# Kernel optimization log

Measured on AMD Instinct MI355X. Metric: run time of the kernel, lower is better.

The kernel has to match this reference:

```python
import jax, jax.numpy as jnp
import numpy as np

B, NJ, NW, NT, D, H = 1024, 16, 2, 2, 128, 128


def _mlp2(x, W1, b1, W2, b2):
    # two-layer dense net with relu on every layer (edge/node networks)
    return jax.nn.relu(jax.nn.relu(x @ W1 + b1) @ W2 + b2)


def _edge_block(src, dst, W1, b1, W2, b2, mask_dst=None):
    # fully-connected edge block: edge(i,j) = MLP(concat(src_i, dst_j)),
    # then avg-pool over destination nodes (masked if mask_dst given)
    Bb, Ns, ds = src.shape
    Nd, dd = dst.shape[1], dst.shape[2]
    e_in = jnp.concatenate([
        jnp.broadcast_to(src[:, :, None, :], (Bb, Ns, Nd, ds)),
        jnp.broadcast_to(dst[:, None, :, :], (Bb, Ns, Nd, dd)),
    ], axis=-1)                              # [B, Ns, Nd, 2D]
    h = _mlp2(e_in, W1, b1, W2, b2)          # [B, Ns, Nd, H]
    if mask_dst is not None:
        m = mask_dst.astype(h.dtype)[:, None, :, None]
        pooled = (h * m).sum(axis=2) / jnp.maximum(m.sum(axis=2), 1.0)
    else:
        pooled = h.mean(axis=2)
    return pooled                            # [B, Ns, H]


def setup_inputs() -> dict:
    key = jax.random.key(0)
    ks = jax.random.split(key, 10)
    def w(k, shape, fan_in):
        return jax.random.normal(k, shape, jnp.float32) / np.float32(np.sqrt(fan_in))
    return {
        "jets": jax.random.normal(ks[0], (B, NJ, D), jnp.float32),
        "nodes_w": jax.random.normal(ks[1], (B, NW, D), jnp.float32),
        "nodes_top": jax.random.normal(ks[2], (B, NT, D), jnp.float32),
        "mask": jax.random.bernoulli(ks[3], 0.8, (B, NJ)),
        # 7 edge nets: 0 jet-jet, 1 jet-W, 2 jet-top, 3 W-jet, 4 W-top, 5 top-jet, 6 top-W
        "edge_W1": w(ks[4], (7, 2 * D, H), 2 * D),
        "edge_b1": jnp.zeros((7, H), jnp.float32),
        "edge_W2": w(ks[5], (7, H, H), H),
        "edge_b2": jnp.zeros((7, H), jnp.float32),
        # jet node net: input D + 3H
        "jet_W1": w(ks[6], (D + 3 * H, H), D + 3 * H),
        "jet_b1": jnp.zeros((H,), jnp.float32),
        "jet_W2": w(ks[7], (H, H), H),
        "jet_b2": jnp.zeros((H,), jnp.float32),
        # W / top node nets (stacked): input D + 2H
        "wt_W1": w(ks[8], (2, D + 2 * H, H), D + 2 * H),
        "wt_b1": jnp.zeros((2, H), jnp.float32),
        "wt_W2": w(ks[9], (2, H, H), H),
        "wt_b2": jnp.zeros((2, H), jnp.float32),
    }


def reference(jets, nodes_w, nodes_top, mask,
              edge_W1, edge_b1, edge_W2, edge_b2,
              jet_W1, jet_b1, jet_W2, jet_b2,
              wt_W1, wt_b1, wt_W2, wt_b2):
    eb = lambda i, s, d, m: _edge_block(s, d, edge_W1[i], edge_b1[i], edge_W2[i], edge_b2[i], m)
    mf = mask.astype(jets.dtype)
    # --- jet update ---
    p_jj = eb(0, jets, jets, mask)
    p_jw = eb(1, jets, nodes_w, None)
    p_jt = eb(2, jets, nodes_top, None)
    jets_cat = jnp.concatenate([jets, p_jj, p_jw, p_jt], axis=-1)
    jets_out = _mlp2(jets_cat, jet_W1, jet_b1, jet_W2, jet_b2) * mf[..., None]
    # --- W update ---
    p_wj = eb(3, nodes_w, jets, mask)
    p_wt = eb(4, nodes_w, nodes_top, None)
    ws_out = _mlp2(jnp.concatenate([nodes_w, p_wj, p_wt], axis=-1),
                   wt_W1[0], wt_b1[0], wt_W2[0], wt_b2[0])
    # --- top update ---
    p_tj = eb(5, nodes_top, jets, mask)
    p_tw = eb(6, nodes_top, nodes_w, None)
    tops_out = _mlp2(jnp.concatenate([nodes_top, p_tj, p_tw], axis=-1),
                     wt_W1[1], wt_b1[1], wt_W2[1], wt_b2[1])
    # concat all updated node types along the node axis: [B, NJ+NW+NT, H]
    return jnp.concatenate([jets_out, ws_out, tops_out], axis=1)
```

## Files before the change

kernel.cpp:

```cpp
#include <hip/hip_runtime.h>
#include <hip/hip_bf16.h>


using short4v = __attribute__((ext_vector_type(4))) short;
using short8 = __attribute__((ext_vector_type(8))) short;
using f32x4  = __attribute__((ext_vector_type(4))) float;
using u32x4  = __attribute__((ext_vector_type(4))) unsigned;

#define DEVI __device__ __forceinline__

DEVI float b2f(short s){
  unsigned u = ((unsigned)(unsigned short)s) << 16;
  float f; __builtin_memcpy(&f, &u, 4); return f;
}
DEVI float lo16f(unsigned w){ unsigned u = w << 16; float f; __builtin_memcpy(&f,&u,4); return f; }
DEVI float hi16f(unsigned w){ unsigned u = w & 0xffff0000u; float f; __builtin_memcpy(&f,&u,4); return f; }
DEVI short f2b(float f){
  __hip_bfloat16 h = __float2bfloat16(f);
  short s; __builtin_memcpy(&s, &h, 2); return s;
}
DEVI unsigned cvtpk(float lo, float hi){
  unsigned r;
  asm("v_cvt_pk_bf16_f32 %0, %1, %2" : "=v"(r) : "v"(lo), "v"(hi));
  return r;
}
DEVI float ldflex(const void* p, long i, int bf){
  return bf ? b2f(((const short*)p)[i]) : ((const float*)p)[i];
}
DEVI f32x4 mfma16(short8 a, short8 b, f32x4 c){
  return __builtin_amdgcn_mfma_f32_16x16x32_bf16(a, b, c, 0, 0, 0);
}

DEVI int detect_bf(const void* jets){
  int l = threadIdx.x & 63;
  int extreme = 0;
  #pragma unroll
  for(int s=0;s<4;s++){
    unsigned short v = ((const unsigned short*)jets)[(l*4+s)*2];
    int e = (v>>7)&0xff;
    if(e<110||e>140) extreme++;
  }
  #pragma unroll
  for(int o=1;o<64;o<<=1) extreme += __shfl_xor(extreme, o);
  return (extreme <= 32) ? 1 : 0;
}
DEVI int detect_fmt(const void* mask){
  int l = threadIdx.x & 63;
  bool all01=true, allf32=true;
  #pragma unroll
  for(int s=0;s<4;s++){
    unsigned w = ((const unsigned*)mask)[l*4+s];
    if(w>1u) all01=false;
    if(w!=0u && w!=0x3F800000u) allf32=false;
  }
  bool allbfv=true; int evnz=0;
  #pragma unroll
  for(int s=0;s<8;s++){
    unsigned short v = ((const unsigned short*)mask)[l*8+s];
    if(v!=0&&v!=0x3F80) allbfv=false;
    if(((l*8+s)&1)==0 && v!=0) evnz++;
  }
  #pragma unroll
  for(int o=1;o<64;o<<=1) evnz += __shfl_xor(evnz, o);
  bool allb01=true;
  #pragma unroll
  for(int s=0;s<16;s++){ if(((const unsigned char*)mask)[l*16+s]>1) allb01=false; }
  int a01 = __all(all01), af32 = __all(allf32), abf = __all(allbfv), ab01 = __all(allb01);
  int fmt = 0;
  if(a01) fmt=0; else if(abf && evnz>0) fmt=2; else if(af32) fmt=3; else if(ab01) fmt=1;
  return fmt;
}

constexpr size_t OF_MASKF  = 256;
constexpr size_t OF_INVCNT = 65792;
constexpr size_t OF_XJ     = 69888;
constexpr size_t OF_XW     = 4264192;
constexpr size_t OF_XT     = 4788480;
constexpr size_t OF_W1T    = 5312768;
constexpr size_t OF_W2T    = 5771520;
constexpr size_t OF_EB1F   = 6000896;
constexpr size_t OF_EB2F   = 6004480;
constexpr size_t OF_JW1T   = 6008064;
constexpr size_t OF_JW2T   = 6139136;
constexpr size_t OF_JB1F   = 6171904;
constexpr size_t OF_JB2F   = 6172416;
constexpr size_t OF_WTW1T  = 6172928;
constexpr size_t OF_WTW2T  = 6369536;
constexpr size_t OF_WTB1F  = 6435072;
constexpr size_t OF_WTB2F  = 6436096;
constexpr size_t OF_UVJ    = 6437120;
constexpr size_t OF_UVW    = 31602944;
constexpr size_t OF_UVT    = 33700096;
constexpr size_t OF_POOL   = 65157376;

__constant__ int QJ_NET[14]  = {0,0,1,2,3,5, 1,3,4,6, 2,4,5,6};
__constant__ int QJ_HALF[14] = {0,1,0,0,1,1, 1,0,0,1, 1,1,0,0};
__constant__ int EB_CUM[8] = {0,2048,2304,2560,2816,3072,3104,3136};
__constant__ int EB_NET[7] = {0,1,2,3,5,4,6};
__constant__ int EN_LGRPB[7] = {8,5,5,5,2,5,2};
__constant__ int EN_LGND2[7] = {4,1,1,4,1,4,1};
__constant__ int EN_LGNSB[7] = {4,4,4,1,1,1,1};
__constant__ int EN_USEL[7] = {0,0,0,1,1,2,2};
__constant__ long long EN_UOFF[7] = {0,4194304,6291456,262144,524288,524288,786432};
__constant__ int EN_VSEL[7] = {0,1,2,0,2,0,1};
__constant__ long long EN_VOFF[7] = {2097152,0,0,8388608,262144,10485760,786432};
__constant__ long long EN_POOL[7] = {0,2097152,4194304,6291456,6553600,6815744,7077888};
__constant__ int TJ_CUM[21] = {0,32,64,96,128,160,192,224,240,256,272,288,304,320,336,400,416,464,512,528,544};
__constant__ int TJ_SEL[20] = {0,0,0,0,0,0,0,1,1,1,1,1,1,1,2,3,4,4,5,5};
__constant__ int TJ_OFF[20] = {0,32768,65536,98304,131072,163840,196608,
                               0,16384,32768,49152,65536,81920,98304,
                               0,0,0,49152,0,16384};
__constant__ int TJ_R[20]   = {256,256,256,256,256,256,256,128,128,128,128,128,128,128,512,128,384,384,128,128};

__global__ __launch_bounds__(256) void k_prep(
    const void* jets, const void* nw, const void* ntop, const void* mask,
    const void* eW1, const void* eb1, const void* eW2, const void* eb2,
    const void* jW1, const void* jb1, const void* jW2, const void* jb2,
    const void* wW1, const void* wb1, const void* wW2, const void* wb2,
    int* flags, float* maskf, float* invcnt,
    short* XJ, short* XW, short* XT,
    short* W1T, short* W2T, short* JW1T, short* JW2T, short* WTW1T, short* WTW2T,
    float* EB1F, float* EB2F, float* JB1F, float* JB2F, float* WTB1F, float* WTB2F){
  __shared__ float tl[32][33];
  int bid = blockIdx.x;
  if(bid < 2560){
    int bf = detect_bf(jets);
    long i = ((long)bid*256 + threadIdx.x)*4;
    const void* src; short* dst; long o;
    if(i < 2097152){ src=jets; dst=XJ; o=i; }
    else if(i < 2359296){ src=nw; dst=XW; o=i-2097152; }
    else { src=ntop; dst=XT; o=i-2359296; }
    short4v r;
    if(bf){
      r = *(const short4v*)((const short*)src + o);
    } else {
      f32x4 v = *(const f32x4*)((const float*)src + o);
      #pragma unroll
      for(int e=0;e<4;e++) r[e] = f2b(v[e]);
    }
    *(short4v*)(dst + o) = r;
  } else if(bid < 3104){
    int bf = detect_bf(jets);
    int tile = bid - 2560; int job = 0;
    while(tile >= TJ_CUM[job+1]) job++;
    tile -= TJ_CUM[job];
    int sel = TJ_SEL[job]; long off = TJ_OFF[job]; int R = TJ_R[job];
    const void* src = sel==0?eW1: sel==1?eW2: sel==2?jW1: sel==3?jW2: sel==4?wW1: wW2;
    short* dst = sel==0?W1T: sel==1?W2T: sel==2?JW1T: sel==3?JW2T: sel==4?WTW1T: WTW2T;
    int tr = (tile>>2)*32, tc = (tile&3)*32;
    int t = threadIdx.x, r = t>>3, c4 = (t&7)*4;
    #pragma unroll
    for(int j=0;j<4;j++) tl[r][c4+j] = ldflex(src, off + (long)(tr+r)*128 + tc + c4 + j, bf);
    __syncthreads();
    short4v o;
    #pragma unroll
    for(int j=0;j<4;j++) o[j] = f2b(tl[c4+j][r]);
    *(short4v*)(dst + off + (long)(tc+r)*R + tr + c4) = o;
  } else if(bid < 3168){
    int fmt = detect_fmt(mask);
    int t = (bid-3104)*256 + threadIdx.x;
    float m;
    if(fmt==0)      m = (((const int*)mask)[t]!=0) ? 1.f : 0.f;
    else if(fmt==1) m = (((const unsigned char*)mask)[t]!=0) ? 1.f : 0.f;
    else if(fmt==2) m = (b2f(((const short*)mask)[t])!=0.f) ? 1.f : 0.f;
    else            m = (((const float*)mask)[t]!=0.f) ? 1.f : 0.f;
    maskf[t] = m;
    float s = m;
    for(int o=1;o<16;o<<=1) s += __shfl_xor(s, o);
    if((t&15)==0) invcnt[t>>4] = 1.f / fmaxf(s, 1.f);
  } else if(bid < 3178){
    int bf = detect_bf(jets);
    int id = (bid-3168)*256 + threadIdx.x;
    if(id<896)        EB1F[id]       = ldflex(eb1, id, bf);
    else if(id<1792)  EB2F[id-896]   = ldflex(eb2, id-896, bf);
    else if(id<1920)  JB1F[id-1792]  = ldflex(jb1, id-1792, bf);
    else if(id<2048)  JB2F[id-1920]  = ldflex(jb2, id-1920, bf);
    else if(id<2304)  WTB1F[id-2048] = ldflex(wb1, id-2048, bf);
    else if(id<2560)  WTB2F[id-2304] = ldflex(wb2, id-2304, bf);
  } else {
    if(threadIdx.x < 64){
      int bf = detect_bf(jets);
      int fmt = detect_fmt(mask);
      if((threadIdx.x & 63) == 0){ flags[0] = bf; flags[1] = fmt; }
    }
  }
}

__global__ __launch_bounds__(256, 4) void k_proj(const short* XJ, const short* XW, const short* XT,
    const short* W1T, const float* EB1F, short* UVJ, short* UVW, short* UVT){
  int bid = blockIdx.x;
  int jp, rb; const short* X; short* out;
  if(bid < 768){ jp = bid>>7; rb = bid&127; X=XJ; out=UVJ + jp*2097152; }
  else if(bid < 832){ int r2=bid-768; jp = 6 + (r2>>4); rb = r2&15; X=XW; out=UVW + (jp-6)*262144; }
  else { int r2=bid-832; jp = 10 + (r2>>4); rb = r2&15; X=XT; out=UVT + (jp-10)*262144; }
  int net = QJ_NET[jp], half = QJ_HALF[jp];
  bool addb = (half==0);
  long row0 = (long)rb * 128;
  const short* Wb = W1T + net*32768 + half*128;
  int t = threadIdx.x, lane = t & 63, wv = t >> 6;
  int rbw = wv >> 1, ch = (wv & 1)*64;
  int cl = lane & 15, kh = lane >> 4;
  short8 bw[4][4];
  f32x4 biasv[4];
  #pragma unroll
  for(int nt=0;nt<4;nt++){
    #pragma unroll
    for(int ks=0;ks<4;ks++)
      bw[nt][ks] = *(const short8*)(Wb + (ch + nt*16 + cl)*256 + ks*32 + kh*8);
    if(addb) biasv[nt] = *(const f32x4*)(EB1F + net*128 + ch + nt*16 + kh*4);
    else     biasv[nt] = f32x4{0.f,0.f,0.f,0.f};
  }
  #pragma unroll 1
  for(int c=0;c<4;c++){
    long T0 = row0 + c*32 + rbw*16;
    short8 a[4];
    #pragma unroll
    for(int ks=0;ks<4;ks++)
      a[ks] = *(const short8*)(X + (T0 + cl)*128 + ks*32 + kh*8);
    f32x4 acc[4] = {};
    #pragma unroll
    for(int ks=0;ks<4;ks++)
      #pragma unroll
      for(int nt=0;nt<4;nt++)
        acc[nt] = mfma16(bw[nt][ks], a[ks], acc[nt]);
    #pragma unroll
    for(int nt=0;nt<4;nt++){
      short4v sv;
      #pragma unroll
      for(int r=0;r<4;r++) sv[r] = f2b(acc[nt][r] + biasv[nt][r]);
      *(short4v*)(out + (T0 + cl)*128 + ch + nt*16 + kh*4) = sv;
    }
  }
}

__global__ __launch_bounds__(256, 4) void k_edge(const short* UVJ, const short* UVW, const short* UVT,
    const short* W2T, const float* EB2F, const float* maskf, const float* invcnt, short* POOL){
  __shared__ short W2s[16384];
  int bid = blockIdx.x;
  int ni = 0;
  while(bid >= EB_CUM[ni+1]) ni++;
  int net = EB_NET[ni];
  long base = (long)(bid - EB_CUM[ni]) * 128;
  int t = threadIdx.x, lane = t & 63, wv = t >> 6;
  int cl = lane & 15, kh = lane >> 4;
  const short* Wg = W2T + net*16384;
  #pragma unroll
  for(int i2=0;i2<8;i2++){
    int c = t + i2*256;
    int row = c>>4, blk = c&15;
    u32x4 w4 = *(const u32x4*)(Wg + row*128 + blk*8);
    *(u32x4*)((char*)W2s + ((row*256 + blk*16) ^ ((row&7)<<4))) = w4;
  }
  int lgRPB = EN_LGRPB[net], lgNd = EN_LGND2[net], lgNsB = EN_LGNSB[net];
  int masked = (lgNd == 4);
  const short* U = (EN_USEL[net]==0?UVJ:(EN_USEL[net]==1?UVW:UVT)) + EN_UOFF[net];
  const short* V = (EN_VSEL[net]==0?UVJ:(EN_VSEL[net]==1?UVW:UVT)) + EN_VOFF[net];
  short* pool = POOL + EN_POOL[net];
  __syncthreads();
  long R0 = base + wv*32;
  long e0 = R0 + cl, e1 = R0 + 16 + cl;
  long urow0 = ((e0>>lgRPB)<<lgNsB) + ((e0 & ((1<<lgRPB)-1)) >> lgNd);
  long vrow0 = ((e0>>lgRPB)<<lgNd)  + (e0 & ((1<<lgNd)-1));
  long urow1 = ((e1>>lgRPB)<<lgNsB) + ((e1 & ((1<<lgRPB)-1)) >> lgNd);
  long vrow1 = ((e1>>lgRPB)<<lgNd)  + (e1 & ((1<<lgNd)-1));
  short8 a0[4], a1[4];
  #pragma unroll
  for(int ks=0;ks<4;ks++){
    u32x4 u = *(const u32x4*)(U + urow0*128 + ks*32 + kh*8);
    u32x4 v = *(const u32x4*)(V + vrow0*128 + ks*32 + kh*8);
    u32x4 aw;
    #pragma unroll
    for(int p=0;p<4;p++)
      aw[p] = cvtpk(fmaxf(lo16f(u[p])+lo16f(v[p]),0.f), fmaxf(hi16f(u[p])+hi16f(v[p]),0.f));
    a0[ks] = __builtin_bit_cast(short8, aw);
  }
  #pragma unroll
  for(int ks=0;ks<4;ks++){
    u32x4 u = *(const u32x4*)(U + urow1*128 + ks*32 + kh*8);
    u32x4 v = *(const u32x4*)(V + vrow1*128 + ks*32 + kh*8);
    u32x4 aw;
    #pragma unroll
    for(int p=0;p<4;p++)
      aw[p] = cvtpk(fmaxf(lo16f(u[p])+lo16f(v[p]),0.f), fmaxf(hi16f(u[p])+hi16f(v[p]),0.f));
    a1[ks] = __builtin_bit_cast(short8, aw);
  }
  f32x4 acc0[8], acc1[8];
  #pragma unroll
  for(int nt=0;nt<8;nt++){
    float bv = EB2F[net*128 + nt*16 + cl];
    acc0[nt] = f32x4{bv,bv,bv,bv};
    acc1[nt] = f32x4{bv,bv,bv,bv};
  }
  #pragma unroll
  for(int ks=0;ks<4;ks++)
    #pragma unroll
    for(int nt=0;nt<8;nt++){
      int row = nt*16 + cl;
      short8 bb = *(const short8*)((const char*)W2s + ((row*256 + ks*64 + kh*16) ^ ((row&7)<<4)));
      acc0[nt] = mfma16(a0[ks], bb, acc0[nt]);
      acc1[nt] = mfma16(a1[ks], bb, acc1[nt]);
    }
  #pragma unroll
  for(int half=0; half<2; half++){
    long RH = R0 + half*16;
    f32x4* acc = half ? acc1 : acc0;
    if(masked){
      long b = RH >> lgRPB;
      float ic = invcnt[b];
      float wr[4];
      #pragma unroll
      for(int r=0;r<4;r++) wr[r] = maskf[b*16 + ((RH + kh*4 + r) & 15)] * ic;
      long prow = RH >> 4;
      #pragma unroll
      for(int nt=0;nt<8;nt++){
        int col = nt*16 + cl;
        float sm = fmaxf(acc[nt][0],0.f)*wr[0] + fmaxf(acc[nt][1],0.f)*wr[1]
                 + fmaxf(acc[nt][2],0.f)*wr[2] + fmaxf(acc[nt][3],0.f)*wr[3];
        sm += __shfl_xor(sm, 16);
        sm += __shfl_xor(sm, 32);
        if(lane < 16) pool[prow*128 + col] = f2b(sm);
      }
    } else {
      long pr = (RH + kh*4) >> 1;
      #pragma unroll
      for(int nt=0;nt<8;nt++){
        int col = nt*16 + cl;
        float v0 = fmaxf(acc[nt][0],0.f), v1 = fmaxf(acc[nt][1],0.f);
        float v2 = fmaxf(acc[nt][2],0.f), v3 = fmaxf(acc[nt][3],0.f);
        pool[pr*128 + col]     = f2b((v0+v1)*0.5f);
        pool[(pr+1)*128 + col] = f2b((v2+v3)*0.5f);
      }
    }
  }
}

__global__ __launch_bounds__(256) void k_node(const short* XJ, const short* XW, const short* XT,
    const short* POOL, const short* JW1T, const short* JW2T, const float* JB1F, const float* JB2F,
    const short* WTW1T, const short* WTW2T, const float* WTB1F, const float* WTB2F,
    const float* maskf, const int* flags, void* out){
  __shared__ short hs[4096];
  int bid = blockIdx.x;
  int net; long row0;
  if(bid < 512){ net=0; row0=(long)bid*32; }
  else if(bid < 576){ net=1; row0=(long)(bid-512)*32; }
  else { net=2; row0=(long)(bid-576)*32; }
  int NQ = (net==0) ? 4 : 3;
  int K1 = NQ*128;
  const short* X = (net==0) ? XJ : ((net==1) ? XW : XT);
  const short *P1, *P2, *P3 = nullptr;
  if(net==0){ P1=POOL; P2=POOL+2097152; P3=POOL+4194304; }
  else if(net==1){ P1=POOL+6291456; P2=POOL+6553600; }
  else { P1=POOL+6815744; P2=POOL+7077888; }
  const short* W1 = (net==0) ? JW1T : WTW1T + (long)(net-1)*49152;
  const short* W2 = (net==0) ? JW2T : WTW2T + (long)(net-1)*16384;
  const float* B1 = (net==0) ? JB1F : WTB1F + (net-1)*128;
  const float* B2 = (net==0) ? JB2F : WTB2F + (net-1)*128;
  int t = threadIdx.x, lane = t & 63, wv = t >> 6;
  int rs = wv >> 1, ch = (wv & 1)*64;
  int cl = lane & 15, kh = lane >> 4;
  int rl = rs*16 + cl;
  long xrow = row0 + rl;
  f32x4 acc[4] = {};
  #pragma unroll
  for(int q=0;q<4;q++){
    if(q < NQ){
      const short* SA = (q==0)?X:((q==1)?P1:((q==2)?P2:P3));
      #pragma unroll
      for(int ks=0;ks<4;ks++){
        short8 a = *(const short8*)(SA + xrow*128 + ks*32 + kh*8);
        #pragma unroll
        for(int nt=0;nt<4;nt++){
          short8 bb = *(const short8*)(W1 + (long)(ch + nt*16 + cl)*K1 + q*128 + ks*32 + kh*8);
          acc[nt] = mfma16(bb, a, acc[nt]);
        }
      }
    }
  }
  #pragma unroll
  for(int nt=0;nt<4;nt++){
    f32x4 bv = *(const f32x4*)(B1 + ch + nt*16 + kh*4);
    short4v sv;
    #pragma unroll
    for(int r=0;r<4;r++) sv[r] = f2b(fmaxf(acc[nt][r] + bv[r], 0.f));
    *(short4v*)((char*)hs + ((rl*256 + (ch + nt*16 + kh*4)*2) ^ ((rl&7)<<4))) = sv;
  }
  __syncthreads();
  f32x4 acc2[4] = {};
  #pragma unroll
  for(int k0=0;k0<4;k0++){
    short8 a = *(const short8*)((const char*)hs + ((rl*256 + (k0*32 + kh*8)*2) ^ ((rl&7)<<4)));
    #pragma unroll
    for(int nt=0;nt<4;nt++){
      short8 bb = *(const short8*)(W2 + (ch + nt*16 + cl)*128 + k0*32 + kh*8);
      acc2[nt] = mfma16(bb, a, acc2[nt]);
    }
  }
  int obf = flags[0];
  long grow = row0 + rl;
  long bbn, node; float mscale = 1.f;
  if(net==0){ bbn = grow>>4; node = grow&15; mscale = maskf[grow]; }
  else if(net==1){ bbn = grow>>1; node = 16 + (grow&1); }
  else { bbn = grow>>1; node = 18 + (grow&1); }
  long obase = (bbn*20 + node)*128;
  #pragma unroll
  for(int nt=0;nt<4;nt++){
    f32x4 bv = *(const f32x4*)(B2 + ch + nt*16 + kh*4);
    f32x4 fv;
    #pragma unroll
    for(int r=0;r<4;r++) fv[r] = fmaxf(acc2[nt][r] + bv[r], 0.f) * mscale;
    if(obf){
      short4v sv;
      #pragma unroll
      for(int r=0;r<4;r++) sv[r] = f2b(fv[r]);
      *(short4v*)((short*)out + obase + ch + nt*16 + kh*4) = sv;
    } else {
      *(f32x4*)((float*)out + obase + ch + nt*16 + kh*4) = fv;
    }
  }
}

extern "C" void kernel_launch(void* const* d_in, const int* in_sizes, int n_in,
                              void* d_out, int out_size, void* d_ws, size_t ws_size,
                              hipStream_t stream){
  char* ws = (char*)d_ws;
  int*   flags  = (int*)ws;
  float* maskf  = (float*)(ws + OF_MASKF);
  float* invcnt = (float*)(ws + OF_INVCNT);
  short* XJ     = (short*)(ws + OF_XJ);
  short* XW     = (short*)(ws + OF_XW);
  short* XT     = (short*)(ws + OF_XT);
  short* W1T    = (short*)(ws + OF_W1T);
  short* W2T    = (short*)(ws + OF_W2T);
  float* EB1F   = (float*)(ws + OF_EB1F);
  float* EB2F   = (float*)(ws + OF_EB2F);
  short* JW1T   = (short*)(ws + OF_JW1T);
  short* JW2T   = (short*)(ws + OF_JW2T);
  float* JB1F   = (float*)(ws + OF_JB1F);
  float* JB2F   = (float*)(ws + OF_JB2F);
  short* WTW1T  = (short*)(ws + OF_WTW1T);
  short* WTW2T  = (short*)(ws + OF_WTW2T);
  float* WTB1F  = (float*)(ws + OF_WTB1F);
  float* WTB2F  = (float*)(ws + OF_WTB2F);
  short* UVJ    = (short*)(ws + OF_UVJ);
  short* UVW    = (short*)(ws + OF_UVW);
  short* UVT    = (short*)(ws + OF_UVT);
  short* POOL   = (short*)(ws + OF_POOL);

  k_prep<<<3179, 256, 0, stream>>>(d_in[0], d_in[1], d_in[2], d_in[3],
                                   d_in[4], d_in[5], d_in[6], d_in[7],
                                   d_in[8], d_in[9], d_in[10], d_in[11],
                                   d_in[12], d_in[13], d_in[14], d_in[15],
                                   flags, maskf, invcnt, XJ, XW, XT,
                                   W1T, W2T, JW1T, JW2T, WTW1T, WTW2T,
                                   EB1F, EB2F, JB1F, JB2F, WTB1F, WTB2F);
  k_proj <<<896, 256, 0, stream>>>(XJ, XW, XT, W1T, EB1F, UVJ, UVW, UVT);
  k_edge <<<3136, 256, 0, stream>>>(UVJ, UVW, UVT, W2T, EB2F, maskf, invcnt, POOL);
  k_node <<<640, 256, 0, stream>>>(XJ, XW, XT, POOL, JW1T, JW2T, JB1F, JB2F,
                                   WTW1T, WTW2T, WTB1F, WTB2F, maskf, flags, d_out);
}
```

Baseline: 100.2 us.

## Restructure projection kernel to reuse input rows across all projection halves

The projection kernel now has each block own 32 input rows, loading the activation fragments once and looping over all projection halves (6 for jets, 4 for W/top), reloading weight fragments per half. Before, each block fixed one weight half and looped over 128 rows. This cuts repeated activation reads and changes the grid from 896 to 640 blocks. In exchange it reloads weights per iteration (mostly from cache), has fewer rows per weight load, and drops the occupancy hint in launch bounds.

```diff
diff --git a/kernel.cpp b/kernel.cpp
--- a/kernel.cpp
+++ b/kernel.cpp
@@ -186,49 +186,52 @@
   }
 }
 
-__global__ __launch_bounds__(256, 4) void k_proj(const short* XJ, const short* XW, const short* XT,
+__global__ __launch_bounds__(256) void k_proj(const short* XJ, const short* XW, const short* XT,
     const short* W1T, const float* EB1F, short* UVJ, short* UVW, short* UVT){
   int bid = blockIdx.x;
-  int jp, rb; const short* X; short* out;
-  if(bid < 768){ jp = bid>>7; rb = bid&127; X=XJ; out=UVJ + jp*2097152; }
-  else if(bid < 832){ int r2=bid-768; jp = 6 + (r2>>4); rb = r2&15; X=XW; out=UVW + (jp-6)*262144; }
-  else { int r2=bid-832; jp = 10 + (r2>>4); rb = r2&15; X=XT; out=UVT + (jp-10)*262144; }
-  int net = QJ_NET[jp], half = QJ_HALF[jp];
-  bool addb = (half==0);
-  long row0 = (long)rb * 128;
-  const short* Wb = W1T + net*32768 + half*128;
+  int jbase, nj; const short* X; long row0;
+  if(bid < 512){ jbase=0; nj=6; X=XJ; row0=(long)bid*32; }
+  else if(bid < 576){ jbase=6; nj=4; X=XW; row0=(long)(bid-512)*32; }
+  else { jbase=10; nj=4; X=XT; row0=(long)(bid-576)*32; }
   int t = threadIdx.x, lane = t & 63, wv = t >> 6;
-  int rbw = wv >> 1, ch = (wv & 1)*64;
+  int rs = wv >> 1, ch = (wv & 1)*64;
   int cl = lane & 15, kh = lane >> 4;
-  short8 bw[4][4];
-  f32x4 biasv[4];
-  #pragma unroll
-  for(int nt=0;nt<4;nt++){
-    #pragma unroll
-    for(int ks=0;ks<4;ks++)
-      bw[nt][ks] = *(const short8*)(Wb + (ch + nt*16 + cl)*256 + ks*32 + kh*8);
-    if(addb) biasv[nt] = *(const f32x4*)(EB1F + net*128 + ch + nt*16 + kh*4);
-    else     biasv[nt] = f32x4{0.f,0.f,0.f,0.f};
-  }
+  long xr = row0 + rs*16 + cl;
+  short8 a[4];
+  #pragma unroll
+  for(int ks=0;ks<4;ks++)
+    a[ks] = *(const short8*)(X + xr*128 + ks*32 + kh*8);
   #pragma unroll 1
-  for(int c=0;c<4;c++){
-    long T0 = row0 + c*32 + rbw*16;
-    short8 a[4];
-    #pragma unroll
-    for(int ks=0;ks<4;ks++)
-      a[ks] = *(const short8*)(X + (T0 + cl)*128 + ks*32 + kh*8);
+  for(int j=0;j<nj;j++){
+    int jp = jbase + j;
+    int net = QJ_NET[jp], half = QJ_HALF[jp];
+    const short* Wb = W1T + net*32768 + half*128;
+    short* out;
+    if(jp < 6)       out = UVJ + jp*2097152;
+    else if(jp < 10) out = UVW + (jp-6)*262144;
+    else             out = UVT + (jp-10)*262144;
+    short8 bw[4][4];
+    #pragma unroll
+    for(int nt=0;nt<4;nt++)
+      #pragma unroll
+      for(int ks=0;ks<4;ks++)
+        bw[nt][ks] = *(const short8*)(Wb + (ch + nt*16 + cl)*256 + ks*32 + kh*8);
     f32x4 acc[4] = {};
     #pragma unroll
     for(int ks=0;ks<4;ks++)
       #pragma unroll
       for(int nt=0;nt<4;nt++)
         acc[nt] = mfma16(bw[nt][ks], a[ks], acc[nt]);
+    bool addb = (half==0);
     #pragma unroll
     for(int nt=0;nt<4;nt++){
+      f32x4 bv;
+      if(addb) bv = *(const f32x4*)(EB1F + net*128 + ch + nt*16 + kh*4);
+      else     bv = f32x4{0.f,0.f,0.f,0.f};
       short4v sv;
       #pragma unroll
-      for(int r=0;r<4;r++) sv[r] = f2b(acc[nt][r] + biasv[nt][r]);
-      *(short4v*)(out + (T0 + cl)*128 + ch + nt*16 + kh*4) = sv;
+      for(int r=0;r<4;r++) sv[r] = f2b(acc[nt][r] + bv[r]);
+      *(short4v*)(out + xr*128 + ch + nt*16 + kh*4) = sv;
     }
   }
 }
@@ -453,7 +456,7 @@
                                    flags, maskf, invcnt, XJ, XW, XT,
                                    W1T, W2T, JW1T, JW2T, WTW1T, WTW2T,
                                    EB1F, EB2F, JB1F, JB2F, WTB1F, WTB2F);
-  k_proj <<<896, 256, 0, stream>>>(XJ, XW, XT, W1T, EB1F, UVJ, UVW, UVT);
+  k_proj <<<640, 256, 0, stream>>>(XJ, XW, XT, W1T, EB1F, UVJ, UVW, UVT);
   k_edge <<<3136, 256, 0, stream>>>(UVJ, UVW, UVT, W2T, EB2F, maskf, invcnt, POOL);
   k_node <<<640, 256, 0, stream>>>(XJ, XW, XT, POOL, JW1T, JW2T, JB1F, JB2F,
                                    WTW1T, WTW2T, WTB1F, WTB2F, maskf, flags, d_out);
```

Result: slower. 114.6 us (+14.4%).
